# Kernel optimization log

Hardware: AMD Instinct MI355X
Metric: run time of the kernel (lower is better)

Reference implementation:

```python
import jax, jax.numpy as jnp
import numpy as np

N = 2_000_000
SH_C0 = 0.282095  # Y_0^0
SH_C1 = 0.488603  # Y_1^m


def setup_inputs() -> dict:
    key = jax.random.key(0)
    k1, k2, k3, k4 = jax.random.split(key, 4)
    positions = jax.random.normal(k1, (N, 3), dtype=jnp.float32)
    colors = jax.random.uniform(k2, (N, 3), dtype=jnp.float32)
    alphas = jnp.ones((N,), dtype=jnp.float32)
    R = jax.random.normal(k3, (N, 3, 3), dtype=jnp.float32)
    S = jax.random.normal(k4, (N, 3, 3), dtype=jnp.float32)
    return {"positions": positions, "colors": colors, "alphas": alphas, "R": R, "S": S}


def _sh_coeffs(colors):
    # colors: [N, 3] -> sh: [N, 4] (band-0 constant + band-1 scaled channels)
    l0 = jnp.full_like(colors[:, 0:1], SH_C0)
    l1_1 = colors[:, 1:2] * SH_C1
    l1_0 = colors[:, 0:1] * SH_C1
    l1_1n = colors[:, 2:3] * SH_C1
    return jnp.concatenate([l0, l1_1, l1_0, l1_1n], axis=1)


def reference(positions, colors, alphas, R, S):
    # Sigma = R (S S^T) R^T, per point, all [N,3,3]
    S_sq = jnp.einsum("nij,nkj->nik", S, S)          # S @ S^T
    cov = jnp.einsum("nij,njk,nlk->nil", R, S_sq, R)  # R @ S_sq @ R^T
    sh = _sh_coeffs(colors)
    return (positions, cov, alphas, sh)
```

## Files before the change

### kernel.cpp

```cpp
#include <hip/hip_runtime.h>


#define SH_C0 0.282095f
#define SH_C1 0.488603f

__global__ __launch_bounds__(256) void gs_kernel(
    const float* __restrict__ pos,
    const float* __restrict__ col,
    const float* __restrict__ alp,
    const float* __restrict__ Rm,
    const float* __restrict__ Sm,
    float* __restrict__ out_pos,
    float* __restrict__ out_cov,
    float* __restrict__ out_alp,
    float* __restrict__ out_sh,
    int n)
{
    int i = blockIdx.x * blockDim.x + threadIdx.x;
    if (i >= n) return;

    out_pos[3 * i + 0] = pos[3 * i + 0];
    out_pos[3 * i + 1] = pos[3 * i + 1];
    out_pos[3 * i + 2] = pos[3 * i + 2];

    out_alp[i] = alp[i];

    float c0 = col[3 * i + 0];
    float c1 = col[3 * i + 1];
    float c2 = col[3 * i + 2];
    out_sh[4 * i + 0] = SH_C0;
    out_sh[4 * i + 1] = c1 * SH_C1;
    out_sh[4 * i + 2] = c0 * SH_C1;
    out_sh[4 * i + 3] = c2 * SH_C1;

    float r[9], s[9];
#pragma unroll
    for (int k = 0; k < 9; ++k) r[k] = Rm[9 * i + k];
#pragma unroll
    for (int k = 0; k < 9; ++k) s[k] = Sm[9 * i + k];

    float t[9];
#pragma unroll
    for (int a = 0; a < 3; ++a) {
#pragma unroll
        for (int b = 0; b < 3; ++b) {
            t[3 * a + b] = r[3 * a + 0] * s[0 + b]
                         + r[3 * a + 1] * s[3 + b]
                         + r[3 * a + 2] * s[6 + b];
        }
    }

#pragma unroll
    for (int a = 0; a < 3; ++a) {
#pragma unroll
        for (int b = 0; b < 3; ++b) {
            out_cov[9 * i + 3 * a + b] = t[3 * a + 0] * t[3 * b + 0]
                                       + t[3 * a + 1] * t[3 * b + 1]
                                       + t[3 * a + 2] * t[3 * b + 2];
        }
    }
}

extern "C" void kernel_launch(void* const* d_in, const int* in_sizes, int n_in,
                              void* d_out, int out_size, void* d_ws, size_t ws_size,
                              hipStream_t stream) {
    const float* pos = (const float*)d_in[0];
    const float* col = (const float*)d_in[1];
    const float* alp = (const float*)d_in[2];
    const float* Rm  = (const float*)d_in[3];
    const float* Sm  = (const float*)d_in[4];

    int n = in_sizes[0] / 3;

    float* out = (float*)d_out;
    float* out_pos = out;
    float* out_cov = out + 3 * n;
    float* out_alp = out + 12 * n;
    float* out_sh  = out + 13 * n;

    int block = 256;
    int grid = (n + block - 1) / block;
    gs_kernel<<<grid, block, 0, stream>>>(pos, col, alp, Rm, Sm,
                                          out_pos, out_cov, out_alp, out_sh, n);
}
```

Before: 279.5 us.

## Stage AoS inputs through LDS with vectorized coalesced loads and nontemporal stores

Loads each block's R, S and color tiles into shared memory with 16-byte vector loads, computes the covariance from LDS, and writes results back through LDS so global stores are coalesced vectors. Pass-through copies of positions and alphas become vectorized block-wide copies. Outputs use nontemporal stores to avoid polluting cache. Adds about 21KB of LDS per block and extra barriers.

```diff
diff --git a/kernel.cpp b/kernel.cpp
--- a/kernel.cpp
+++ b/kernel.cpp
@@ -1,10 +1,13 @@
 #include <hip/hip_runtime.h>
 
 
+typedef float v4f __attribute__((ext_vector_type(4)));
+
 #define SH_C0 0.282095f
 #define SH_C1 0.488603f
+#define BLK 256
 
-__global__ __launch_bounds__(256) void gs_kernel(
+__global__ __launch_bounds__(BLK) void gs_kernel(
     const float* __restrict__ pos,
     const float* __restrict__ col,
     const float* __restrict__ alp,
@@ -16,48 +19,93 @@
     float* __restrict__ out_sh,
     int n)
 {
-    int i = blockIdx.x * blockDim.x + threadIdx.x;
-    if (i >= n) return;
+    __shared__ float ldsR[BLK * 9];
+    __shared__ float ldsS[BLK * 9];
+    __shared__ float ldsC[BLK * 3];
 
-    out_pos[3 * i + 0] = pos[3 * i + 0];
-    out_pos[3 * i + 1] = pos[3 * i + 1];
-    out_pos[3 * i + 2] = pos[3 * i + 2];
+    const int t  = threadIdx.x;
+    const int b  = blockIdx.x;
+    const int p0 = b * BLK;
+    const int cnt = min(BLK, n - p0);
 
-    out_alp[i] = alp[i];
+    const int nrs4 = (cnt * 9) / 4;
+    const int nc4  = (cnt * 3) / 4;
+    const v4f* Rv = (const v4f*)(Rm + (size_t)p0 * 9);
+    const v4f* Sv = (const v4f*)(Sm + (size_t)p0 * 9);
+    const v4f* Cv = (const v4f*)(col + (size_t)p0 * 3);
+    v4f* ldsRv = (v4f*)ldsR;
+    v4f* ldsSv = (v4f*)ldsS;
+    v4f* ldsCv = (v4f*)ldsC;
+    for (int k = t; k < nrs4; k += BLK) {
+        ldsRv[k] = Rv[k];
+        ldsSv[k] = Sv[k];
+    }
+    for (int k = t; k < nc4; k += BLK) ldsCv[k] = Cv[k];
+    for (int k = nrs4 * 4 + t; k < cnt * 9; k += BLK) {
+        ldsR[k] = Rm[(size_t)p0 * 9 + k];
+        ldsS[k] = Sm[(size_t)p0 * 9 + k];
+    }
+    for (int k = nc4 * 4 + t; k < cnt * 3; k += BLK)
+        ldsC[k] = col[(size_t)p0 * 3 + k];
+    __syncthreads();
 
-    float c0 = col[3 * i + 0];
-    float c1 = col[3 * i + 1];
-    float c2 = col[3 * i + 2];
-    out_sh[4 * i + 0] = SH_C0;
-    out_sh[4 * i + 1] = c1 * SH_C1;
-    out_sh[4 * i + 2] = c0 * SH_C1;
-    out_sh[4 * i + 3] = c2 * SH_C1;
+    float covv[9];
+    const bool active = (t < cnt);
+    if (active) {
+        float r[9], s[9], tt[9];
+#pragma unroll
+        for (int k = 0; k < 9; ++k) r[k] = ldsR[9 * t + k];
+#pragma unroll
+        for (int k = 0; k < 9; ++k) s[k] = ldsS[9 * t + k];
+#pragma unroll
+        for (int a = 0; a < 3; ++a)
+#pragma unroll
+            for (int c = 0; c < 3; ++c)
+                tt[3 * a + c] = r[3 * a + 0] * s[0 + c]
+                              + r[3 * a + 1] * s[3 + c]
+                              + r[3 * a + 2] * s[6 + c];
+#pragma unroll
+        for (int a = 0; a < 3; ++a)
+#pragma unroll
+            for (int c = 0; c < 3; ++c)
+                covv[3 * a + c] = tt[3 * a + 0] * tt[3 * c + 0]
+                                + tt[3 * a + 1] * tt[3 * c + 1]
+                                + tt[3 * a + 2] * tt[3 * c + 2];
 
-    float r[9], s[9];
-#pragma unroll
-    for (int k = 0; k < 9; ++k) r[k] = Rm[9 * i + k];
-#pragma unroll
-    for (int k = 0; k < 9; ++k) s[k] = Sm[9 * i + k];
-
-    float t[9];
-#pragma unroll
-    for (int a = 0; a < 3; ++a) {
-#pragma unroll
-        for (int b = 0; b < 3; ++b) {
-            t[3 * a + b] = r[3 * a + 0] * s[0 + b]
-                         + r[3 * a + 1] * s[3 + b]
-                         + r[3 * a + 2] * s[6 + b];
-        }
+        float c0 = ldsC[3 * t + 0], c1 = ldsC[3 * t + 1], c2 = ldsC[3 * t + 2];
+        v4f sh = {SH_C0, c1 * SH_C1, c0 * SH_C1, c2 * SH_C1};
+        __builtin_nontemporal_store(sh, (v4f*)(out_sh + (size_t)(p0 + t) * 4));
     }
 
+    __syncthreads();
+    if (active) {
 #pragma unroll
-    for (int a = 0; a < 3; ++a) {
-#pragma unroll
-        for (int b = 0; b < 3; ++b) {
-            out_cov[9 * i + 3 * a + b] = t[3 * a + 0] * t[3 * b + 0]
-                                       + t[3 * a + 1] * t[3 * b + 1]
-                                       + t[3 * a + 2] * t[3 * b + 2];
-        }
+        for (int k = 0; k < 9; ++k) ldsR[9 * t + k] = covv[k];
+    }
+    __syncthreads();
+
+    v4f* Ov = (v4f*)(out_cov + (size_t)p0 * 9);
+    for (int k = t; k < nrs4; k += BLK)
+        __builtin_nontemporal_store(ldsRv[k], Ov + k);
+    for (int k = nrs4 * 4 + t; k < cnt * 9; k += BLK)
+        out_cov[(size_t)p0 * 9 + k] = ldsR[k];
+
+    {
+        const int np4 = (cnt * 3) / 4;
+        const v4f* Pv = (const v4f*)(pos + (size_t)p0 * 3);
+        v4f*      OPv = (v4f*)(out_pos + (size_t)p0 * 3);
+        for (int k = t; k < np4; k += BLK)
+            __builtin_nontemporal_store(Pv[k], OPv + k);
+        for (int k = np4 * 4 + t; k < cnt * 3; k += BLK)
+            out_pos[(size_t)p0 * 3 + k] = pos[(size_t)p0 * 3 + k];
+
+        const int na4 = cnt / 4;
+        const v4f* Av = (const v4f*)(alp + (size_t)p0);
+        v4f*      OAv = (v4f*)(out_alp + (size_t)p0);
+        for (int k = t; k < na4; k += BLK)
+            __builtin_nontemporal_store(Av[k], OAv + k);
+        for (int k = na4 * 4 + t; k < cnt; k += BLK)
+            out_alp[(size_t)p0 + k] = alp[(size_t)p0 + k];
     }
 }
 
@@ -74,12 +122,11 @@
 
     float* out = (float*)d_out;
     float* out_pos = out;
-    float* out_cov = out + 3 * n;
-    float* out_alp = out + 12 * n;
-    float* out_sh  = out + 13 * n;
+    float* out_cov = out + (size_t)3 * n;
+    float* out_alp = out + (size_t)12 * n;
+    float* out_sh  = out + (size_t)13 * n;
 
-    int block = 256;
-    int grid = (n + block - 1) / block;
-    gs_kernel<<<grid, block, 0, stream>>>(pos, col, alp, Rm, Sm,
-                                          out_pos, out_cov, out_alp, out_sh, n);
+    int grid = (n + BLK - 1) / BLK;
+    gs_kernel<<<grid, BLK, 0, stream>>>(pos, col, alp, Rm, Sm,
+                                        out_pos, out_cov, out_alp, out_sh, n);
 }
```

New measurement: 286.6 us. 2.5% more time.
